# Kernel tuning notes

Measured on AMD Instinct MI355X. Metric: run time of the kernel, lower is better.

The kernel has to match this reference:

```python
import jax, jax.numpy as jnp
import numpy as np

COMMITMENT_COST = 0.25
NUM_EMBEDDINGS = 8192
EMBEDDING_DIM = 256


def setup_inputs() -> dict:
    key = jax.random.key(0)
    k1, k2 = jax.random.split(key)
    inputs = jax.random.normal(k1, (32, 256, EMBEDDING_DIM), dtype=jnp.float32)
    codebook = jax.random.normal(k2, (NUM_EMBEDDINGS, EMBEDDING_DIM), dtype=jnp.float32)
    # match nn.Embedding init: N(0,1) then L2-normalize rows
    codebook = codebook / jnp.linalg.norm(codebook, axis=1, keepdims=True)
    return {"inputs": inputs, "codebook": codebook}


def reference(inputs, codebook):
    B, K, D = inputs.shape
    flat = inputs.reshape(-1, D).astype(jnp.float32)  # [N, D], N = B*K
    N = flat.shape[0]

    distances = (
        jnp.sum(flat * flat, axis=1, keepdims=True)
        + jnp.sum(codebook * codebook, axis=1)
        - 2.0 * flat @ codebook.T
    )
    indices = jnp.argmin(distances, axis=1)  # [N]

    # codebook lookup (equivalent to one-hot @ codebook)
    quantized = codebook[indices].reshape(B, K, D)

    e_latent_loss = jnp.mean((jax.lax.stop_gradient(quantized) - inputs) ** 2)
    q_latent_loss = jnp.mean((quantized - jax.lax.stop_gradient(inputs)) ** 2)
    loss = q_latent_loss + COMMITMENT_COST * e_latent_loss

    # straight-through estimator
    quantized_ste = inputs + jax.lax.stop_gradient(quantized - inputs)

    # perplexity from codebook usage histogram (== mean of one-hot encodings)
    counts = jnp.zeros((NUM_EMBEDDINGS,), dtype=jnp.float32).at[indices].add(1.0)
    avg_probs = counts / N
    perplexity = jnp.exp(-jnp.sum(avg_probs * jnp.log(avg_probs + 1e-10)))

    return quantized_ste, loss, perplexity
```

## Files before the change

kernel.cpp:

```cpp
#include <hip/hip_runtime.h>
#include <math.h>

#define NTOK 8192
#define NEMB 8192
#define DIM  256

typedef _Float16 f16x8 __attribute__((ext_vector_type(8)));
typedef _Float16 f16x4 __attribute__((ext_vector_type(4)));
typedef float    f32x4 __attribute__((ext_vector_type(4)));

__global__ __launch_bounds__(256) void convert_kernel(
        const float* __restrict__ X, const float* __restrict__ C,
        _Float16* __restrict__ Xh, _Float16* __restrict__ Ch,
        float* __restrict__ cnorm, float* __restrict__ xnorm,
        unsigned long long* __restrict__ keys, int* __restrict__ counts) {
    const bool isC = (blockIdx.y != 0);
    if (isC && blockIdx.x < 8) {
        ((int4*)counts)[blockIdx.x * 256 + threadIdx.x] = make_int4(0, 0, 0, 0);
    }
    if (!isC && blockIdx.x < 8) {
        int4 ff = make_int4(-1, -1, -1, -1);
        ((int4*)keys)[blockIdx.x * 512 + threadIdx.x * 2]     = ff;
        ((int4*)keys)[blockIdx.x * 512 + threadIdx.x * 2 + 1] = ff;
    }
    const float* src = isC ? C : X;
    _Float16* dst = isC ? Ch : Xh;
    size_t t = (size_t)blockIdx.x * 256 + threadIdx.x;
    float4 x = *(const float4*)&src[t * 4];
    f16x4 h;
    h[0] = (_Float16)x.x; h[1] = (_Float16)x.y;
    h[2] = (_Float16)x.z; h[3] = (_Float16)x.w;
    *(f16x4*)&dst[t * 4] = h;
    float s = x.x * x.x + x.y * x.y + x.z * x.z + x.w * x.w;
    #pragma unroll
    for (int off = 32; off >= 1; off >>= 1) s += __shfl_xor(s, off);
    if ((threadIdx.x & 63) == 0) {
        if (isC) cnorm[t >> 6] = s; else xnorm[t >> 6] = s;
    }
}

__device__ __forceinline__ int swz(int row) { return (row + (row >> 2)) & 3; }

template<int N>
__device__ __forceinline__ void wait_vmcnt() {
    asm volatile("s_waitcnt vmcnt(%0)" :: "n"(N) : "memory");
}

__device__ __forceinline__ void stage_k32(
        const _Float16* __restrict__ Ag, const _Float16* __restrict__ Bg,
        _Float16* buf, int t) {
    #pragma unroll
    for (int c = 0; c < 4; ++c) {
        int gr  = c * 256 + t;
        int row = gr >> 2;
        int kg  = (gr & 3) ^ swz(row);
        __builtin_amdgcn_global_load_lds(
            (const __attribute__((address_space(1))) void*)(Ag + (size_t)row * DIM + kg * 8),
            (__attribute__((address_space(3))) void*)(buf + (size_t)gr * 8), 16, 0, 0);
    }
    #pragma unroll
    for (int c = 0; c < 2; ++c) {
        int gr  = c * 256 + t;
        int row = gr >> 2;
        int kg  = (gr & 3) ^ swz(row);
        __builtin_amdgcn_global_load_lds(
            (const __attribute__((address_space(1))) void*)(Bg + (size_t)row * DIM + kg * 8),
            (__attribute__((address_space(3))) void*)(buf + 8192 + (size_t)gr * 8), 16, 0, 0);
    }
}

__device__ __forceinline__ void compute_k32(
        const _Float16* buf, f32x4 (&acc)[8][4],
        int wm, int wn, int lrow, int g) {
    const _Float16* Ab = buf;
    const _Float16* Bb = buf + 8192;
    f16x8 af[8], bf_[4];
    #pragma unroll
    for (int tm = 0; tm < 8; ++tm) {
        int row = wm + tm * 16 + lrow;
        af[tm] = *(const f16x8*)&Ab[(row * 4 + (g ^ swz(row))) * 8];
    }
    #pragma unroll
    for (int tn = 0; tn < 4; ++tn) {
        int row = wn + tn * 16 + lrow;
        bf_[tn] = *(const f16x8*)&Bb[(row * 4 + (g ^ swz(row))) * 8];
    }
    __builtin_amdgcn_s_setprio(1);
    #pragma unroll
    for (int tm = 0; tm < 8; ++tm)
        #pragma unroll
        for (int tn = 0; tn < 4; ++tn)
            acc[tm][tn] = __builtin_amdgcn_mfma_f32_16x16x32_f16(
                af[tm], bf_[tn], acc[tm][tn], 0, 0, 0);
    __builtin_amdgcn_s_setprio(0);
}

__global__ __launch_bounds__(256, 2) void mfma_argmin_kernel(
        const _Float16* __restrict__ Xh, const _Float16* __restrict__ Ch,
        const float* __restrict__ cnorm,
        unsigned long long* __restrict__ keys) {
    __shared__ __align__(16) _Float16 lds[36864];

    const int t = threadIdx.x;
    const int wid = t >> 6, lane = t & 63;
    const int tb0 = blockIdx.x * 128;
    const int cb0 = blockIdx.y * 256;
    const int wm = (wid >> 1) * 128;
    const int wn = (wid & 1) * 64;
    const int lrow = lane & 15;
    const int g = lane >> 4;

    f32x4 acc[8][4];
    #pragma unroll
    for (int a = 0; a < 8; ++a)
        #pragma unroll
        for (int b = 0; b < 4; ++b) acc[a][b] = (f32x4)0.0f;

    const _Float16* Ag = Ch + (size_t)cb0 * DIM;
    const _Float16* Bg = Xh + (size_t)tb0 * DIM;

    stage_k32(Ag,      Bg,      lds,         t);
    stage_k32(Ag + 32, Bg + 32, lds + 12288, t);

#define PHASE(P, LAST)                                                        \
    do {                                                                      \
        wait_vmcnt<(LAST) ? 0 : 6>();                                         \
        __builtin_amdgcn_s_barrier();                                         \
        __builtin_amdgcn_sched_barrier(0);                                    \
        if ((P) + 2 < 8)                                                      \
            stage_k32(Ag + ((P) + 2) * 32, Bg + ((P) + 2) * 32,               \
                      lds + (((P) + 2) % 3) * 12288, t);                      \
        compute_k32(lds + ((P) % 3) * 12288, acc, wm, wn, lrow, g);           \
        __builtin_amdgcn_sched_barrier(0);                                    \
    } while (0)

    PHASE(0, false); PHASE(1, false); PHASE(2, false); PHASE(3, false);
    PHASE(4, false); PHASE(5, false); PHASE(6, false); PHASE(7, true);
#undef PHASE

    float cn[32];
    #pragma unroll
    for (int tm = 0; tm < 8; ++tm)
        #pragma unroll
        for (int reg = 0; reg < 4; ++reg)
            cn[tm * 4 + reg] = cnorm[cb0 + wm + tm * 16 + g * 4 + reg];

    float* cmb_v = (float*)lds;
    int*   cmb_i = (int*)((float*)lds + 256);

    #pragma unroll
    for (int tn = 0; tn < 4; ++tn) {
        float bv = 1e30f; int bi = 0x7fffffff;
        #pragma unroll
        for (int tm = 0; tm < 8; ++tm) {
            #pragma unroll
            for (int reg = 0; reg < 4; ++reg) {
                float d = fmaf(-2.0f, acc[tm][tn][reg], cn[tm * 4 + reg]);
                int code = cb0 + wm + tm * 16 + g * 4 + reg;
                if (d < bv) { bv = d; bi = code; }
            }
        }
        #pragma unroll
        for (int off = 16; off <= 32; off <<= 1) {
            float ov = __shfl_xor(bv, off);
            int   oi = __shfl_xor(bi, off);
            if (ov < bv || (ov == bv && oi < bi)) { bv = ov; bi = oi; }
        }
        if (g == 0) {
            int tl = wn + tn * 16 + lrow;
            cmb_v[tl * 2 + (wid >> 1)] = bv;
            cmb_i[tl * 2 + (wid >> 1)] = bi;
        }
    }
    __syncthreads();
    if (t < 128) {
        float v0 = cmb_v[t * 2], v1 = cmb_v[t * 2 + 1];
        int   i0 = cmb_i[t * 2], i1 = cmb_i[t * 2 + 1];
        bool tk = (v1 < v0) || (v1 == v0 && i1 < i0);
        float bv = tk ? v1 : v0;
        int   bi = tk ? i1 : i0;
        unsigned long long key =
            ((unsigned long long)__builtin_bit_cast(unsigned, bv + 64.0f) << 32)
            | (unsigned)bi;
        atomicMin(&keys[tb0 + t], key);
    }
}

__global__ __launch_bounds__(256) void gather_kernel(
        const float* __restrict__ C, const unsigned long long* __restrict__ keys,
        const float* __restrict__ xnorm, int* __restrict__ counts,
        float* __restrict__ out, float* __restrict__ psum) {
    __shared__ int idx_lds[32];
    const int m0 = blockIdx.x * 32;
    const int t = threadIdx.x;
    if (t < 32) {
        unsigned long long k = keys[m0 + t];
        int bi  = (int)(unsigned)k;
        float d = __builtin_bit_cast(float, (unsigned)(k >> 32)) - 64.0f;
        idx_lds[t] = bi;
        atomicAdd(&counts[bi], 1);
        float lt = d + xnorm[m0 + t];
        #pragma unroll
        for (int off = 1; off < 32; off <<= 1) lt += __shfl_xor(lt, off);
        if (t == 0) psum[blockIdx.x] = lt;
    }
    __syncthreads();
    const int wid = t >> 6, lane = t & 63;
    #pragma unroll
    for (int r = 0; r < 8; ++r) {
        int token = m0 + wid * 8 + r;
        int e = idx_lds[wid * 8 + r];
        float4 q = *(const float4*)&C[(size_t)e * DIM + lane * 4];
        *(float4*)&out[(size_t)token * DIM + lane * 4] = q;
    }
}

__global__ __launch_bounds__(1024) void finalize_kernel(
        const int* __restrict__ counts, const float* __restrict__ psum,
        float* __restrict__ out) {
    const int t = threadIdx.x;
    double local = 0.0;
    #pragma unroll
    for (int i = 0; i < 8; ++i) {
        int e = t + i * 1024;
        float p = (float)counts[e] * (1.0f / (float)NTOK);
        local += (double)(p * logf(p + 1e-10f));
    }
    float ls = (t < 256) ? psum[t] : 0.0f;
    #pragma unroll
    for (int off = 32; off >= 1; off >>= 1) {
        local += __shfl_xor(local, off);
        ls    += __shfl_xor(ls, off);
    }
    __shared__ double she[16];
    __shared__ float  shs[16];
    int lane = t & 63, wid = t >> 6;
    if (lane == 0) { she[wid] = local; shs[wid] = ls; }
    __syncthreads();
    if (t == 0) {
        double ent = 0.0; float ssq = 0.0f;
        #pragma unroll
        for (int w = 0; w < 16; ++w) { ent += she[w]; ssq += shs[w]; }
        out[(size_t)NTOK * DIM]     = 1.25f * ssq / (float)((size_t)NTOK * DIM);
        out[(size_t)NTOK * DIM + 1] = expf((float)(-ent));
    }
}

extern "C" void kernel_launch(void* const* d_in, const int* in_sizes, int n_in,
                              void* d_out, int out_size, void* d_ws, size_t ws_size,
                              hipStream_t stream) {
    const float* X = (const float*)d_in[0];
    const float* C = (const float*)d_in[1];
    float* out = (float*)d_out;

    char* ws = (char*)d_ws;
    size_t o = 0;
    _Float16* Xh = (_Float16*)(ws + o); o += (size_t)NTOK * DIM * 2;
    _Float16* Ch = (_Float16*)(ws + o); o += (size_t)NEMB * DIM * 2;
    float* cnorm = (float*)(ws + o); o += (size_t)NEMB * 4;
    float* xnorm = (float*)(ws + o); o += (size_t)NTOK * 4;
    unsigned long long* keys = (unsigned long long*)(ws + o); o += (size_t)NTOK * 8;
    int* counts  = (int*)(ws + o);   o += (size_t)NEMB * 4;
    float* psum  = (float*)(ws + o);

    convert_kernel<<<dim3(NTOK * DIM / 4 / 256, 2), 256, 0, stream>>>(
        X, C, Xh, Ch, cnorm, xnorm, keys, counts);
    mfma_argmin_kernel<<<dim3(NTOK / 128, NEMB / 256), 256, 0, stream>>>(
        Xh, Ch, cnorm, keys);
    gather_kernel<<<256, 256, 0, stream>>>(
        C, keys, xnorm, counts, out, psum);
    finalize_kernel<<<1, 1024, 0, stream>>>(counts, psum, out);
}
```

Baseline: 119.2 us.

## Load token operand directly from global into registers, shrink LDS staging to codebook only

The token (B) operand no longer goes through LDS staging. Each wave loads its B fragments straight from global memory into a double-buffered register array, one k-step ahead, and only the codebook tile goes through LDS, which shrinks from 72KB to 48KB. The A fragment loads are split into two halves to reduce register pressure, and the vmcnt wait counts are retuned to cover the mixed async-to-LDS and register loads. This removes LDS traffic and space for B, which may allow better occupancy. The cost is uncoalesced 16-byte per-lane global loads and more VGPRs for the prefetched B registers.

```diff
diff --git a/kernel.cpp b/kernel.cpp
--- a/kernel.cpp
+++ b/kernel.cpp
@@ -46,9 +46,8 @@
     asm volatile("s_waitcnt vmcnt(%0)" :: "n"(N) : "memory");
 }
 
-__device__ __forceinline__ void stage_k32(
-        const _Float16* __restrict__ Ag, const _Float16* __restrict__ Bg,
-        _Float16* buf, int t) {
+__device__ __forceinline__ void stage_a32(
+        const _Float16* __restrict__ Ag, _Float16* buf, int t) {
     #pragma unroll
     for (int c = 0; c < 4; ++c) {
         int gr  = c * 256 + t;
@@ -58,48 +57,43 @@
             (const __attribute__((address_space(1))) void*)(Ag + (size_t)row * DIM + kg * 8),
             (__attribute__((address_space(3))) void*)(buf + (size_t)gr * 8), 16, 0, 0);
     }
-    #pragma unroll
-    for (int c = 0; c < 2; ++c) {
-        int gr  = c * 256 + t;
-        int row = gr >> 2;
-        int kg  = (gr & 3) ^ swz(row);
-        __builtin_amdgcn_global_load_lds(
-            (const __attribute__((address_space(1))) void*)(Bg + (size_t)row * DIM + kg * 8),
-            (__attribute__((address_space(3))) void*)(buf + 8192 + (size_t)gr * 8), 16, 0, 0);
-    }
-}
-
-__device__ __forceinline__ void compute_k32(
-        const _Float16* buf, f32x4 (&acc)[8][4],
-        int wm, int wn, int lrow, int g) {
-    const _Float16* Ab = buf;
-    const _Float16* Bb = buf + 8192;
-    f16x8 af[8], bf_[4];
-    #pragma unroll
-    for (int tm = 0; tm < 8; ++tm) {
-        int row = wm + tm * 16 + lrow;
-        af[tm] = *(const f16x8*)&Ab[(row * 4 + (g ^ swz(row))) * 8];
-    }
-    #pragma unroll
-    for (int tn = 0; tn < 4; ++tn) {
-        int row = wn + tn * 16 + lrow;
-        bf_[tn] = *(const f16x8*)&Bb[(row * 4 + (g ^ swz(row))) * 8];
-    }
-    __builtin_amdgcn_s_setprio(1);
-    #pragma unroll
-    for (int tm = 0; tm < 8; ++tm)
-        #pragma unroll
-        for (int tn = 0; tn < 4; ++tn)
-            acc[tm][tn] = __builtin_amdgcn_mfma_f32_16x16x32_f16(
-                af[tm], bf_[tn], acc[tm][tn], 0, 0, 0);
-    __builtin_amdgcn_s_setprio(0);
+}
+
+template<int Q>
+__device__ __forceinline__ void load_b(
+        const _Float16* const (&bbase)[4], f16x8 (&dst)[4]) {
+    #pragma unroll
+    for (int tn = 0; tn < 4; ++tn)
+        dst[tn] = *(const f16x8*)&bbase[tn][Q * 32];
+}
+
+__device__ __forceinline__ void compute_a(
+        const _Float16* Abuf, const f16x8 (&bf)[4], f32x4 (&acc)[8][4],
+        int wm, int lrow, int g) {
+    #pragma unroll
+    for (int h = 0; h < 2; ++h) {
+        f16x8 af[4];
+        #pragma unroll
+        for (int i = 0; i < 4; ++i) {
+            int row = wm + (h * 4 + i) * 16 + lrow;
+            af[i] = *(const f16x8*)&Abuf[(row * 4 + (g ^ swz(row))) * 8];
+        }
+        __builtin_amdgcn_s_setprio(1);
+        #pragma unroll
+        for (int i = 0; i < 4; ++i)
+            #pragma unroll
+            for (int tn = 0; tn < 4; ++tn)
+                acc[h * 4 + i][tn] = __builtin_amdgcn_mfma_f32_16x16x32_f16(
+                    af[i], bf[tn], acc[h * 4 + i][tn], 0, 0, 0);
+        __builtin_amdgcn_s_setprio(0);
+    }
 }
 
 __global__ __launch_bounds__(256, 2) void mfma_argmin_kernel(
         const _Float16* __restrict__ Xh, const _Float16* __restrict__ Ch,
         const float* __restrict__ cnorm,
         unsigned long long* __restrict__ keys) {
-    __shared__ __align__(16) _Float16 lds[36864];
+    __shared__ __align__(16) _Float16 lds[24576];
 
     const int t = threadIdx.x;
     const int wid = t >> 6, lane = t & 63;
@@ -117,25 +111,33 @@
         for (int b = 0; b < 4; ++b) acc[a][b] = (f32x4)0.0f;
 
     const _Float16* Ag = Ch + (size_t)cb0 * DIM;
-    const _Float16* Bg = Xh + (size_t)tb0 * DIM;
-
-    stage_k32(Ag,      Bg,      lds,         t);
-    stage_k32(Ag + 32, Bg + 32, lds + 12288, t);
-
-#define PHASE(P, LAST)                                                        \
+
+    const _Float16* bbase[4];
+    #pragma unroll
+    for (int tn = 0; tn < 4; ++tn)
+        bbase[tn] = Xh + (size_t)(tb0 + wn + tn * 16 + lrow) * DIM + g * 8;
+
+    f16x8 bf[2][4];
+
+    stage_a32(Ag,      lds,        t);
+    stage_a32(Ag + 32, lds + 8192, t);
+    load_b<0>(bbase, bf[0]);
+
+#define PHASE(P, WAITN, LAST)                                                 \
     do {                                                                      \
-        wait_vmcnt<(LAST) ? 0 : 6>();                                         \
+        wait_vmcnt<WAITN>();                                                  \
         __builtin_amdgcn_s_barrier();                                         \
         __builtin_amdgcn_sched_barrier(0);                                    \
         if ((P) + 2 < 8)                                                      \
-            stage_k32(Ag + ((P) + 2) * 32, Bg + ((P) + 2) * 32,               \
-                      lds + (((P) + 2) % 3) * 12288, t);                      \
-        compute_k32(lds + ((P) % 3) * 12288, acc, wm, wn, lrow, g);           \
+            stage_a32(Ag + ((P) + 2) * 32, lds + (((P) + 2) % 3) * 8192, t);  \
+        if (!(LAST)) load_b<((P) + 1) & 7>(bbase, bf[((P) + 1) & 1]);         \
+        compute_a(lds + ((P) % 3) * 8192, bf[(P) & 1], acc, wm, lrow, g);     \
         __builtin_amdgcn_sched_barrier(0);                                    \
     } while (0)
 
-    PHASE(0, false); PHASE(1, false); PHASE(2, false); PHASE(3, false);
-    PHASE(4, false); PHASE(5, false); PHASE(6, false); PHASE(7, true);
+    PHASE(0,  8, false); PHASE(1, 12, false); PHASE(2, 12, false);
+    PHASE(3, 12, false); PHASE(4, 12, false); PHASE(5, 12, false);
+    PHASE(6, 12, false); PHASE(7,  8, true);
 #undef PHASE
 
     float cn[32];
```

Result: slower. 130.4 us (+9.4%).

## Split argmin GEMM block across eight waves with smaller per-wave tiles

Applied to the files above, without the earlier changes.

The MFMA argmin kernel now launches 512 threads (8 waves) per block instead of 256. Each wave computes a 64x64 tile rather than 128x64, which halves the accumulator registers per wave and raises launch bounds to 4 blocks per SM. Staging loads are spread over more threads, with separate A/B LDS regions and a 4-way cross-wave argmin reduction. The aim is more latency hiding through occupancy, at the cost of fewer MFMAs per LDS fragment load and more reduction and barrier overhead.

```diff
diff --git a/kernel.cpp b/kernel.cpp
--- a/kernel.cpp
+++ b/kernel.cpp
@@ -48,111 +48,111 @@
 
 __device__ __forceinline__ void stage_k32(
         const _Float16* __restrict__ Ag, const _Float16* __restrict__ Bg,
-        _Float16* buf, int t) {
-    #pragma unroll
-    for (int c = 0; c < 4; ++c) {
-        int gr  = c * 256 + t;
+        _Float16* bufA, _Float16* bufB, int t) {
+    #pragma unroll
+    for (int c = 0; c < 2; ++c) {
+        int gr  = c * 512 + t;
         int row = gr >> 2;
         int kg  = (gr & 3) ^ swz(row);
         __builtin_amdgcn_global_load_lds(
             (const __attribute__((address_space(1))) void*)(Ag + (size_t)row * DIM + kg * 8),
-            (__attribute__((address_space(3))) void*)(buf + (size_t)gr * 8), 16, 0, 0);
-    }
-    #pragma unroll
-    for (int c = 0; c < 2; ++c) {
-        int gr  = c * 256 + t;
+            (__attribute__((address_space(3))) void*)(bufA + (size_t)gr * 8), 16, 0, 0);
+    }
+    {
+        int gr  = t;
         int row = gr >> 2;
         int kg  = (gr & 3) ^ swz(row);
         __builtin_amdgcn_global_load_lds(
             (const __attribute__((address_space(1))) void*)(Bg + (size_t)row * DIM + kg * 8),
-            (__attribute__((address_space(3))) void*)(buf + 8192 + (size_t)gr * 8), 16, 0, 0);
+            (__attribute__((address_space(3))) void*)(bufB + (size_t)gr * 8), 16, 0, 0);
     }
 }
 
 __device__ __forceinline__ void compute_k32(
-        const _Float16* buf, f32x4 (&acc)[8][4],
+        const _Float16* Abuf, const _Float16* Bbuf, f32x4 (&acc)[4][4],
         int wm, int wn, int lrow, int g) {
-    const _Float16* Ab = buf;
-    const _Float16* Bb = buf + 8192;
-    f16x8 af[8], bf_[4];
-    #pragma unroll
-    for (int tm = 0; tm < 8; ++tm) {
-        int row = wm + tm * 16 + lrow;
-        af[tm] = *(const f16x8*)&Ab[(row * 4 + (g ^ swz(row))) * 8];
-    }
-    #pragma unroll
-    for (int tn = 0; tn < 4; ++tn) {
-        int row = wn + tn * 16 + lrow;
-        bf_[tn] = *(const f16x8*)&Bb[(row * 4 + (g ^ swz(row))) * 8];
+    f16x8 af[4], bf_[4];
+    #pragma unroll
+    for (int i = 0; i < 4; ++i) {
+        int row = wm + i * 16 + lrow;
+        af[i] = *(const f16x8*)&Abuf[(row * 4 + (g ^ swz(row))) * 8];
+    }
+    #pragma unroll
+    for (int j = 0; j < 4; ++j) {
+        int row = wn + j * 16 + lrow;
+        bf_[j] = *(const f16x8*)&Bbuf[(row * 4 + (g ^ swz(row))) * 8];
     }
     __builtin_amdgcn_s_setprio(1);
     #pragma unroll
-    for (int tm = 0; tm < 8; ++tm)
-        #pragma unroll
-        for (int tn = 0; tn < 4; ++tn)
-            acc[tm][tn] = __builtin_amdgcn_mfma_f32_16x16x32_f16(
-                af[tm], bf_[tn], acc[tm][tn], 0, 0, 0);
+    for (int i = 0; i < 4; ++i)
+        #pragma unroll
+        for (int j = 0; j < 4; ++j)
+            acc[i][j] = __builtin_amdgcn_mfma_f32_16x16x32_f16(
+                af[i], bf_[j], acc[i][j], 0, 0, 0);
     __builtin_amdgcn_s_setprio(0);
 }
 
-__global__ __launch_bounds__(256, 2) void mfma_argmin_kernel(
+__global__ __launch_bounds__(512, 4) void mfma_argmin_kernel(
         const _Float16* __restrict__ Xh, const _Float16* __restrict__ Ch,
         const float* __restrict__ cnorm,
         unsigned long long* __restrict__ keys) {
     __shared__ __align__(16) _Float16 lds[36864];
+    _Float16* const ldsB = lds + 24576;
 
     const int t = threadIdx.x;
     const int wid = t >> 6, lane = t & 63;
     const int tb0 = blockIdx.x * 128;
     const int cb0 = blockIdx.y * 256;
-    const int wm = (wid >> 1) * 128;
+    const int wm = (wid >> 1) * 64;
     const int wn = (wid & 1) * 64;
     const int lrow = lane & 15;
     const int g = lane >> 4;
 
-    f32x4 acc[8][4];
-    #pragma unroll
-    for (int a = 0; a < 8; ++a)
+    f32x4 acc[4][4];
+    #pragma unroll
+    for (int a = 0; a < 4; ++a)
         #pragma unroll
         for (int b = 0; b < 4; ++b) acc[a][b] = (f32x4)0.0f;
 
     const _Float16* Ag = Ch + (size_t)cb0 * DIM;
     const _Float16* Bg = Xh + (size_t)tb0 * DIM;
 
-    stage_k32(Ag,      Bg,      lds,         t);
-    stage_k32(Ag + 32, Bg + 32, lds + 12288, t);
-
-#define PHASE(P, LAST)                                                        \
+    stage_k32(Ag,      Bg,      lds,        ldsB,        t);
+    stage_k32(Ag + 32, Bg + 32, lds + 8192, ldsB + 4096, t);
+
+#define PHASE(P, WAITN)                                                       \
     do {                                                                      \
-        wait_vmcnt<(LAST) ? 0 : 6>();                                         \
+        wait_vmcnt<WAITN>();                                                  \
         __builtin_amdgcn_s_barrier();                                         \
         __builtin_amdgcn_sched_barrier(0);                                    \
         if ((P) + 2 < 8)                                                      \
             stage_k32(Ag + ((P) + 2) * 32, Bg + ((P) + 2) * 32,               \
-                      lds + (((P) + 2) % 3) * 12288, t);                      \
-        compute_k32(lds + ((P) % 3) * 12288, acc, wm, wn, lrow, g);           \
+                      lds + (((P) + 2) % 3) * 8192,                           \
+                      ldsB + (((P) + 2) % 3) * 4096, t);                      \
+        compute_k32(lds + ((P) % 3) * 8192, ldsB + ((P) % 3) * 4096,          \
+                    acc, wm, wn, lrow, g);                                    \
         __builtin_amdgcn_sched_barrier(0);                                    \
     } while (0)
 
-    PHASE(0, false); PHASE(1, false); PHASE(2, false); PHASE(3, false);
-    PHASE(4, false); PHASE(5, false); PHASE(6, false); PHASE(7, true);
+    PHASE(0, 3); PHASE(1, 3); PHASE(2, 3); PHASE(3, 3);
+    PHASE(4, 3); PHASE(5, 3); PHASE(6, 3); PHASE(7, 0);
 #undef PHASE
 
-    float cn[32];
-    #pragma unroll
-    for (int tm = 0; tm < 8; ++tm)
+    float cn[16];
+    #pragma unroll
+    for (int tm = 0; tm < 4; ++tm)
         #pragma unroll
         for (int reg = 0; reg < 4; ++reg)
             cn[tm * 4 + reg] = cnorm[cb0 + wm + tm * 16 + g * 4 + reg];
 
     float* cmb_v = (float*)lds;
-    int*   cmb_i = (int*)((float*)lds + 256);
+    int*   cmb_i = (int*)((float*)lds + 512);
 
     #pragma unroll
     for (int tn = 0; tn < 4; ++tn) {
         float bv = 1e30f; int bi = 0x7fffffff;
         #pragma unroll
-        for (int tm = 0; tm < 8; ++tm) {
+        for (int tm = 0; tm < 4; ++tm) {
             #pragma unroll
             for (int reg = 0; reg < 4; ++reg) {
                 float d = fmaf(-2.0f, acc[tm][tn][reg], cn[tm * 4 + reg]);
@@ -168,17 +168,19 @@
         }
         if (g == 0) {
             int tl = wn + tn * 16 + lrow;
-            cmb_v[tl * 2 + (wid >> 1)] = bv;
-            cmb_i[tl * 2 + (wid >> 1)] = bi;
+            cmb_v[tl * 4 + (wid >> 1)] = bv;
+            cmb_i[tl * 4 + (wid >> 1)] = bi;
         }
     }
     __syncthreads();
     if (t < 128) {
-        float v0 = cmb_v[t * 2], v1 = cmb_v[t * 2 + 1];
-        int   i0 = cmb_i[t * 2], i1 = cmb_i[t * 2 + 1];
-        bool tk = (v1 < v0) || (v1 == v0 && i1 < i0);
-        float bv = tk ? v1 : v0;
-        int   bi = tk ? i1 : i0;
+        float bv = cmb_v[t * 4]; int bi = cmb_i[t * 4];
+        #pragma unroll
+        for (int w = 1; w < 4; ++w) {
+            float ov = cmb_v[t * 4 + w];
+            int   oi = cmb_i[t * 4 + w];
+            if (ov < bv || (ov == bv && oi < bi)) { bv = ov; bi = oi; }
+        }
         unsigned long long key =
             ((unsigned long long)__builtin_bit_cast(unsigned, bv + 64.0f) << 32)
             | (unsigned)bi;
@@ -265,7 +267,7 @@
 
     convert_kernel<<<dim3(NTOK * DIM / 4 / 256, 2), 256, 0, stream>>>(
         X, C, Xh, Ch, cnorm, xnorm, keys, counts);
-    mfma_argmin_kernel<<<dim3(NTOK / 128, NEMB / 256), 256, 0, stream>>>(
+    mfma_argmin_kernel<<<dim3(NTOK / 128, NEMB / 256), 512, 0, stream>>>(
         Xh, Ch, cnorm, keys);
     gather_kernel<<<256, 256, 0, stream>>>(
         C, keys, xnorm, counts, out, psum);
```

Result: no change. 117.2 us (median of 2 runs) (-1.7%).
